# Kernel optimization log

Hardware: AMD Instinct MI355X
Metric: run time of the kernel (lower is better)

## Reference

```python
import jax, jax.numpy as jnp
import numpy as np

B, D3, DQ, H, UNITS, SK = 32, 1024, 1024, 1024, 1024, 1024


def setup_inputs() -> dict:
    key = jax.random.key(0)
    ks = jax.random.split(key, 11)
    return {
        "K": jax.random.normal(ks[0], (B, SK, UNITS), jnp.float32),
        "Q": jax.random.normal(ks[1], (B, DQ, D3), jnp.float32),
        "M": jax.random.normal(ks[2], (B, D3, D3), jnp.float32),
        "ht": jax.random.normal(ks[3], (B, D3, H), jnp.float32),
        "Wp": jax.random.normal(ks[4], (D3, DQ), jnp.float32) * 0.02,
        "bp": jax.random.normal(ks[5], (D3,), jnp.float32) * 0.02,
        "W3": jax.random.normal(ks[6], (D3, D3), jnp.float32) * 0.02,
        "W4": jax.random.normal(ks[7], (D3, D3), jnp.float32) * 0.02,
        "b3": jax.random.normal(ks[8], (D3,), jnp.float32) * 0.02,
        "Wd": jax.random.normal(ks[9], (H + D3, UNITS), jnp.float32) * 0.02,
        "bd": jax.random.normal(ks[10], (UNITS,), jnp.float32) * 0.02,
    }


def reference(K, Q, M, ht, Wp, bp, W3, W4, b3, Wd, bd):
    # q = Wp @ Q + bp  -> (B, d3, d3); bp broadcasts over the last axis
    q = jnp.einsum('ij,bjk->bik', Wp, Q) + bp
    # concat([ht, q], axis=-1) -> (B, d3, h + d3), then fresh Dense(units)
    concat = jnp.concatenate([ht, q], axis=-1)
    mlp = jnp.einsum('bdc,cu->bdu', concat, Wd) + bd  # (B, d3, units)
    # scores = K @ mlp^T, softmax over last axis (computed but unused in the
    # original layer's output -- kept for faithfulness; DCE'd under jit)
    scores = jnp.einsum('bsu,bdu->bsd', K, mlp)       # (B, sK, d3)
    distribution = jax.nn.softmax(scores, axis=-1)
    del distribution
    # Belta = relu(W3 @ M + W4 @ q + b3), gated multiply with q
    Belta = jax.nn.relu(
        jnp.einsum('ij,bjk->bik', W3, M)
        + jnp.einsum('ij,bjk->bik', W4, q)
        + b3
    )
    q_new = Belta * q  # (B, d3, d3)
    return q_new
```

## Files before the change

### kernel.cpp

```cpp
#include <hip/hip_runtime.h>
#include <stdint.h>


#define D_ 1024

typedef __attribute__((ext_vector_type(8))) short short8;
typedef __attribute__((ext_vector_type(4))) float floatx4;
typedef __attribute__((ext_vector_type(4))) unsigned short us4;

#define VMCNT0() asm volatile("s_waitcnt vmcnt(0)" ::: "memory")
#define VMCNT4() asm volatile("s_waitcnt vmcnt(4)" ::: "memory")
#define LGKM0()  asm volatile("s_waitcnt lgkmcnt(0)" ::: "memory")

__device__ __forceinline__ unsigned short f2bf(float f) {
  union { float f; unsigned int u; } v; v.f = f;
  unsigned int u = v.u;
  unsigned int r = (u + 0x7FFFu + ((u >> 16) & 1u)) >> 16;
  return (unsigned short)r;
}

__device__ __forceinline__ float bf2f(unsigned short h) {
  union { unsigned int u; float f; } v; v.u = ((unsigned int)h) << 16;
  return v.f;
}

__device__ __forceinline__ void async_load16(const void* g, void* l) {
  __builtin_amdgcn_global_load_lds(
      (const __attribute__((address_space(1))) unsigned int*)g,
      (__attribute__((address_space(3))) unsigned int*)l, 16, 0, 0);
}

__global__ __launch_bounds__(256) void transpose_cvt2(
    const float* __restrict__ in0, unsigned short* __restrict__ out0,
    const float* __restrict__ in1, unsigned short* __restrict__ out1) {
  __shared__ float tile[64][65];
  const int zz = blockIdx.z;
  const float* in = (zz < 32) ? in0 : in1;
  unsigned short* out = (zz < 32) ? out0 : out1;
  const int b = zz & 31;
  const long base = ((long)b) << 20;
  const int r0 = blockIdx.y * 64, c0 = blockIdx.x * 64;
  const int t = threadIdx.x;
  const int tr = t >> 4, tc4 = (t & 15) * 4;
#pragma unroll
  for (int p = 0; p < 4; ++p) {
    const int row = p * 16 + tr;
    const float4 v = *(const float4*)&in[base + (long)(r0 + row) * D_ + c0 + tc4];
    tile[row][tc4 + 0] = v.x; tile[row][tc4 + 1] = v.y;
    tile[row][tc4 + 2] = v.z; tile[row][tc4 + 3] = v.w;
  }
  __syncthreads();
#pragma unroll
  for (int p = 0; p < 4; ++p) {
    const int c = p * 16 + tr;
    us4 pk;
    pk.x = f2bf(tile[tc4 + 0][c]);
    pk.y = f2bf(tile[tc4 + 1][c]);
    pk.z = f2bf(tile[tc4 + 2][c]);
    pk.w = f2bf(tile[tc4 + 3][c]);
    *(us4*)&out[base + (long)(c0 + c) * D_ + r0 + tc4] = pk;
  }
}

__global__ __launch_bounds__(256) void convert_weights(
    const float* __restrict__ Wp, const float* __restrict__ W3,
    const float* __restrict__ W4, unsigned short* __restrict__ Wpb,
    unsigned short* __restrict__ A2) {
  const int i = blockIdx.x * 256 + threadIdx.x;
  const long e = (long)i * 4;
  const int row = (int)(e >> 10);
  const int col = (int)(e & 1023);
  const float4 a = ((const float4*)Wp)[i];
  us4 pa; pa.x = f2bf(a.x); pa.y = f2bf(a.y); pa.z = f2bf(a.z); pa.w = f2bf(a.w);
  ((us4*)Wpb)[i] = pa;
  const float4 w3 = ((const float4*)W3)[i];
  us4 p3; p3.x = f2bf(w3.x); p3.y = f2bf(w3.y); p3.z = f2bf(w3.z); p3.w = f2bf(w3.w);
  *(us4*)&A2[(long)row * 2048 + col] = p3;
  const float4 w4 = ((const float4*)W4)[i];
  us4 p4; p4.x = f2bf(w4.x); p4.y = f2bf(w4.y); p4.z = f2bf(w4.z); p4.w = f2bf(w4.w);
  *(us4*)&A2[(long)row * 2048 + 1024 + col] = p4;
}

template <int NT, int LDA, bool IS_G2>
__global__ __launch_bounds__(512, 2) void gemm8p(
    const unsigned short* __restrict__ A,
    const unsigned short* __restrict__ B1,
    const unsigned short* __restrict__ B2,
    const float* __restrict__ bias,
    void* __restrict__ outp) {
  __shared__ __align__(16) unsigned short As[2][256 * 64];
  __shared__ __align__(16) unsigned short Bs[2][256 * 64];

  const int lane = threadIdx.x & 63;
  const int w = threadIdx.x >> 6;
  const int wm = (w >> 2) * 128;
  const int wn = (w & 3) * 64;
  const int l15 = lane & 15;
  const int quad = lane >> 4;

  const int bid = blockIdx.x;
  const int swz = (bid & 7) * 64 + (bid >> 3);
  const int b = swz >> 4;
  const int m0 = ((swz >> 2) & 3) * 256;
  const int n0 = (swz & 3) * 256;
  const long bb = ((long)b) << 20;

  const int sr = lane >> 3;
  const int sc = ((lane & 7) ^ sr) * 8;

  const unsigned short* Ag = A + (long)(m0 + w * 16 + sr) * LDA + sc;
  const unsigned short* Bg1 = B1 + bb + (long)(n0 + w * 16 + sr) * D_ + sc;
  const unsigned short* Bg2 =
      B2 ? (B2 + bb + (long)(n0 + w * 16 + sr) * D_ + sc) : (const unsigned short*)0;

  const int kx0 = (quad * 16) ^ ((lane & 7) << 4);
  const int kx1 = (64 + quad * 16) ^ ((lane & 7) << 4);

  floatx4 acc[8][4] = {};

  auto stageAh = [&](int buf, int kt, int h) {
#pragma unroll
    for (int j = 0; j < 2; ++j)
      async_load16(Ag + (long)(h * 128 + j * 8) * LDA + (long)kt * 64,
                   &As[buf][(h * 128 + w * 16 + j * 8) * 64]);
  };
  auto stageBh = [&](int buf, int kt, int h) {
    const unsigned short* bs;
    if constexpr (IS_G2) {
      bs = (kt < 16) ? (Bg1 + (long)kt * 64) : (Bg2 + (long)(kt - 16) * 64);
    } else {
      bs = Bg1 + (long)kt * 64;
    }
#pragma unroll
    for (int j = 0; j < 2; ++j)
      async_load16(bs + (long)(h * 128 + j * 8) * D_,
                   &Bs[buf][(h * 128 + w * 16 + j * 8) * 64]);
  };

  auto ldA = [&](int buf, int fi, int kx) -> short8 {
    return *(const short8*)((const char*)&As[buf][0] +
                            (long)((wm + fi * 16 + l15) * 128 + kx));
  };
  auto ldB = [&](int buf, int fi, int kx) -> short8 {
    return *(const short8*)((const char*)&Bs[buf][0] +
                            (long)((wn + fi * 16 + l15) * 128 + kx));
  };

  stageAh(0, 0, 0); stageAh(0, 0, 1);
  stageBh(0, 0, 0); stageBh(0, 0, 1);
  stageBh(1, 1, 0); stageBh(1, 1, 1);
  VMCNT4();
  __builtin_amdgcn_s_barrier();

  short8 a[4][2], bq[4][2];

  auto tile = [&](int t, int buf) {
#pragma unroll
    for (int r = 0; r < 4; ++r) { a[r][0] = ldA(buf, r, kx0); a[r][1] = ldA(buf, r, kx1); }
#pragma unroll
    for (int c = 0; c < 2; ++c) { bq[c][0] = ldB(buf, c, kx0); bq[c][1] = ldB(buf, c, kx1); }
    if (t + 1 < NT) stageAh(buf ^ 1, t + 1, 0);
    __builtin_amdgcn_s_barrier();
    LGKM0();
    __builtin_amdgcn_sched_barrier(0);
    __builtin_amdgcn_s_setprio(1);
#pragma unroll
    for (int r = 0; r < 4; ++r)
#pragma unroll
      for (int c = 0; c < 2; ++c)
#pragma unroll
        for (int ks = 0; ks < 2; ++ks)
          acc[r][c] = __builtin_amdgcn_mfma_f32_16x16x32_bf16(
              a[r][ks], bq[c][ks], acc[r][c], 0, 0, 0);
    __builtin_amdgcn_s_setprio(0);
    __builtin_amdgcn_s_barrier();

#pragma unroll
    for (int c = 0; c < 2; ++c) { bq[2 + c][0] = ldB(buf, 2 + c, kx0); bq[2 + c][1] = ldB(buf, 2 + c, kx1); }
    if (t + 1 < NT) stageAh(buf ^ 1, t + 1, 1);
    __builtin_amdgcn_s_barrier();
    LGKM0();
    __builtin_amdgcn_sched_barrier(0);
    __builtin_amdgcn_s_setprio(1);
#pragma unroll
    for (int r = 0; r < 4; ++r)
#pragma unroll
      for (int c = 0; c < 2; ++c)
#pragma unroll
        for (int ks = 0; ks < 2; ++ks)
          acc[r][2 + c] = __builtin_amdgcn_mfma_f32_16x16x32_bf16(
              a[r][ks], bq[2 + c][ks], acc[r][2 + c], 0, 0, 0);
    __builtin_amdgcn_s_setprio(0);
    __builtin_amdgcn_s_barrier();

#pragma unroll
    for (int r = 0; r < 4; ++r) { a[r][0] = ldA(buf, 4 + r, kx0); a[r][1] = ldA(buf, 4 + r, kx1); }
    if (t + 2 < NT) stageBh(buf, t + 2, 0);
    __builtin_amdgcn_s_barrier();
    LGKM0();
    __builtin_amdgcn_sched_barrier(0);
    __builtin_amdgcn_s_setprio(1);
#pragma unroll
    for (int r = 0; r < 4; ++r)
#pragma unroll
      for (int c = 0; c < 2; ++c)
#pragma unroll
        for (int ks = 0; ks < 2; ++ks)
          acc[4 + r][2 + c] = __builtin_amdgcn_mfma_f32_16x16x32_bf16(
              a[r][ks], bq[2 + c][ks], acc[4 + r][2 + c], 0, 0, 0);
    __builtin_amdgcn_s_setprio(0);
    __builtin_amdgcn_s_barrier();

    if (t + 2 < NT) stageBh(buf, t + 2, 1);
    __builtin_amdgcn_s_barrier();
    __builtin_amdgcn_s_setprio(1);
#pragma unroll
    for (int r = 0; r < 4; ++r)
#pragma unroll
      for (int c = 0; c < 2; ++c)
#pragma unroll
        for (int ks = 0; ks < 2; ++ks)
          acc[4 + r][c] = __builtin_amdgcn_mfma_f32_16x16x32_bf16(
              a[r][ks], bq[c][ks], acc[4 + r][c], 0, 0, 0);
    __builtin_amdgcn_s_setprio(0);
    if (t < NT - 2) { VMCNT4(); } else { VMCNT0(); }
    __builtin_amdgcn_s_barrier();
  };

#pragma unroll 1
  for (int tt = 0; tt < NT; tt += 2) {
    tile(tt, 0);
    tile(tt + 1, 1);
  }

  if constexpr (!IS_G2) {
    unsigned short* qt = (unsigned short*)outp;
#pragma unroll
    for (int c = 0; c < 4; ++c) {
      const int col = n0 + wn + c * 16 + l15;
      const float bv = bias[col];
#pragma unroll
      for (int r = 0; r < 8; ++r) {
        const int row = m0 + wm + r * 16 + quad * 4;
        const floatx4 v = acc[r][c];
        us4 pk;
        pk.x = f2bf(v.x + bv); pk.y = f2bf(v.y + bv);
        pk.z = f2bf(v.z + bv); pk.w = f2bf(v.w + bv);
        *(us4*)&qt[bb + (long)col * D_ + row] = pk;
      }
    }
  } else {
    float* outv = (float*)outp;
#pragma unroll
    for (int c = 0; c < 4; ++c) {
      const int col = n0 + wn + c * 16 + l15;
      const float bv = bias[col];
#pragma unroll
      for (int r = 0; r < 8; ++r) {
        const int row = m0 + wm + r * 16 + quad * 4;
        const floatx4 v = acc[r][c];
        const us4 qv = *(const us4*)&B2[bb + (long)col * D_ + row];
        outv[bb + (long)(row + 0) * D_ + col] = fmaxf(v.x + bv, 0.0f) * bf2f(qv.x);
        outv[bb + (long)(row + 1) * D_ + col] = fmaxf(v.y + bv, 0.0f) * bf2f(qv.y);
        outv[bb + (long)(row + 2) * D_ + col] = fmaxf(v.z + bv, 0.0f) * bf2f(qv.z);
        outv[bb + (long)(row + 3) * D_ + col] = fmaxf(v.w + bv, 0.0f) * bf2f(qv.w);
      }
    }
  }
}

extern "C" void kernel_launch(void* const* d_in, const int* in_sizes, int n_in,
                              void* d_out, int out_size, void* d_ws, size_t ws_size,
                              hipStream_t stream) {
  const float* Q  = (const float*)d_in[1];
  const float* M  = (const float*)d_in[2];
  const float* Wp = (const float*)d_in[4];
  const float* bp = (const float*)d_in[5];
  const float* W3 = (const float*)d_in[6];
  const float* W4 = (const float*)d_in[7];
  const float* b3 = (const float*)d_in[8];
  float* out = (float*)d_out;

  char* ws = (char*)d_ws;
  unsigned short* qt  = (unsigned short*)(ws);
  unsigned short* Qt  = (unsigned short*)(ws + (64l  << 20));
  unsigned short* Mt  = (unsigned short*)(ws + (128l << 20));
  unsigned short* Wpb = (unsigned short*)(ws + (192l << 20));
  unsigned short* A2  = (unsigned short*)(ws + (194l << 20));

  dim3 tgrid(16, 16, 64);
  transpose_cvt2<<<tgrid, 256, 0, stream>>>(Q, Qt, M, Mt);
  convert_weights<<<1024, 256, 0, stream>>>(Wp, W3, W4, Wpb, A2);

  gemm8p<16, 1024, false><<<dim3(512), dim3(512), 0, stream>>>(
      Wpb, Qt, (const unsigned short*)nullptr, bp, qt);
  gemm8p<32, 2048, true><<<dim3(512), dim3(512), 0, stream>>>(
      A2, Mt, qt, b3, out);
}
```

Measured before the change: 689.1 us.

## Restructure GEMM main loop with ping-pong register fragments and whole-tile prefetch

Replaces the per-tile four-phase schedule with separate low and high A/B register fragment sets. LDS reads for the next quadrant or next k-tile are issued while the MFMAs of the current quadrant run, and quadrant order alternates between even and odd tiles so fragments are reused. Global-to-LDS staging now loads the whole A and B tile for t+2 at once, waiting with vmcnt(8) and then vmcnt(0), instead of staging A for t+1 and B for t+2 in halves. This aims to hide LDS latency behind matrix-core work, at the cost of more registers and a full vmcnt(0) wait in every tile.

```diff
diff --git a/kernel.cpp b/kernel.cpp
--- a/kernel.cpp
+++ b/kernel.cpp
@@ -9,8 +9,23 @@
 typedef __attribute__((ext_vector_type(4))) unsigned short us4;
 
 #define VMCNT0() asm volatile("s_waitcnt vmcnt(0)" ::: "memory")
-#define VMCNT4() asm volatile("s_waitcnt vmcnt(4)" ::: "memory")
+#define VMCNT8() asm volatile("s_waitcnt vmcnt(8)" ::: "memory")
 #define LGKM0()  asm volatile("s_waitcnt lgkmcnt(0)" ::: "memory")
+#define SCHED0() __builtin_amdgcn_sched_barrier(0)
+#define BAR()    __builtin_amdgcn_s_barrier()
+
+#define MQ(ASET, BSET, R0, C0)                                               \
+  do {                                                                       \
+    __builtin_amdgcn_s_setprio(1);                                           \
+    _Pragma("unroll") for (int r_ = 0; r_ < 4; ++r_)                         \
+        _Pragma("unroll") for (int c_ = 0; c_ < 2; ++c_)                     \
+            _Pragma("unroll") for (int k_ = 0; k_ < 2; ++k_)                 \
+                acc[(R0) + r_][(C0) + c_] =                                  \
+                    __builtin_amdgcn_mfma_f32_16x16x32_bf16(                 \
+                        ASET[r_][k_], BSET[c_][k_],                          \
+                        acc[(R0) + r_][(C0) + c_], 0, 0, 0);                 \
+    __builtin_amdgcn_s_setprio(0);                                           \
+  } while (0)
 
 __device__ __forceinline__ unsigned short f2bf(float f) {
   union { float f; unsigned int u; } v; v.f = f;
@@ -82,7 +97,7 @@
 }
 
 template <int NT, int LDA, bool IS_G2>
-__global__ __launch_bounds__(512, 2) void gemm8p(
+__global__ __launch_bounds__(512, 2) void gemmpl(
     const unsigned short* __restrict__ A,
     const unsigned short* __restrict__ B1,
     const unsigned short* __restrict__ B2,
@@ -117,14 +132,19 @@
   const int kx1 = (64 + quad * 16) ^ ((lane & 7) << 4);
 
   floatx4 acc[8][4] = {};
-
-  auto stageAh = [&](int buf, int kt, int h) {
-#pragma unroll
-    for (int j = 0; j < 2; ++j)
-      async_load16(Ag + (long)(h * 128 + j * 8) * LDA + (long)kt * 64,
-                   &As[buf][(h * 128 + w * 16 + j * 8) * 64]);
-  };
-  auto stageBh = [&](int buf, int kt, int h) {
+  short8 aLo[4][2], aHi[4][2], bLo[2][2], bHi[2][2];
+
+  auto stageA = [&](int kt) {
+    unsigned short* dst = &As[kt & 1][0];
+#pragma unroll
+    for (int h = 0; h < 2; ++h)
+#pragma unroll
+      for (int j = 0; j < 2; ++j)
+        async_load16(Ag + (long)(h * 128 + j * 8) * LDA + (long)kt * 64,
+                     dst + (h * 128 + w * 16 + j * 8) * 64);
+  };
+  auto stageB = [&](int kt) {
+    unsigned short* dst = &Bs[kt & 1][0];
     const unsigned short* bs;
     if constexpr (IS_G2) {
       bs = (kt < 16) ? (Bg1 + (long)kt * 64) : (Bg2 + (long)(kt - 16) * 64);
@@ -132,9 +152,11 @@
       bs = Bg1 + (long)kt * 64;
     }
 #pragma unroll
-    for (int j = 0; j < 2; ++j)
-      async_load16(bs + (long)(h * 128 + j * 8) * D_,
-                   &Bs[buf][(h * 128 + w * 16 + j * 8) * 64]);
+    for (int h = 0; h < 2; ++h)
+#pragma unroll
+      for (int j = 0; j < 2; ++j)
+        async_load16(bs + (long)(h * 128 + j * 8) * D_,
+                     dst + (h * 128 + w * 16 + j * 8) * 64);
   };
 
   auto ldA = [&](int buf, int fi, int kx) -> short8 {
@@ -146,91 +168,75 @@
                             (long)((wn + fi * 16 + l15) * 128 + kx));
   };
 
-  stageAh(0, 0, 0); stageAh(0, 0, 1);
-  stageBh(0, 0, 0); stageBh(0, 0, 1);
-  stageBh(1, 1, 0); stageBh(1, 1, 1);
-  VMCNT4();
-  __builtin_amdgcn_s_barrier();
-
-  short8 a[4][2], bq[4][2];
-
-  auto tile = [&](int t, int buf) {
-#pragma unroll
-    for (int r = 0; r < 4; ++r) { a[r][0] = ldA(buf, r, kx0); a[r][1] = ldA(buf, r, kx1); }
-#pragma unroll
-    for (int c = 0; c < 2; ++c) { bq[c][0] = ldB(buf, c, kx0); bq[c][1] = ldB(buf, c, kx1); }
-    if (t + 1 < NT) stageAh(buf ^ 1, t + 1, 0);
-    __builtin_amdgcn_s_barrier();
-    LGKM0();
-    __builtin_amdgcn_sched_barrier(0);
-    __builtin_amdgcn_s_setprio(1);
-#pragma unroll
-    for (int r = 0; r < 4; ++r)
-#pragma unroll
-      for (int c = 0; c < 2; ++c)
-#pragma unroll
-        for (int ks = 0; ks < 2; ++ks)
-          acc[r][c] = __builtin_amdgcn_mfma_f32_16x16x32_bf16(
-              a[r][ks], bq[c][ks], acc[r][c], 0, 0, 0);
-    __builtin_amdgcn_s_setprio(0);
-    __builtin_amdgcn_s_barrier();
-
-#pragma unroll
-    for (int c = 0; c < 2; ++c) { bq[2 + c][0] = ldB(buf, 2 + c, kx0); bq[2 + c][1] = ldB(buf, 2 + c, kx1); }
-    if (t + 1 < NT) stageAh(buf ^ 1, t + 1, 1);
-    __builtin_amdgcn_s_barrier();
-    LGKM0();
-    __builtin_amdgcn_sched_barrier(0);
-    __builtin_amdgcn_s_setprio(1);
-#pragma unroll
-    for (int r = 0; r < 4; ++r)
-#pragma unroll
-      for (int c = 0; c < 2; ++c)
-#pragma unroll
-        for (int ks = 0; ks < 2; ++ks)
-          acc[r][2 + c] = __builtin_amdgcn_mfma_f32_16x16x32_bf16(
-              a[r][ks], bq[2 + c][ks], acc[r][2 + c], 0, 0, 0);
-    __builtin_amdgcn_s_setprio(0);
-    __builtin_amdgcn_s_barrier();
-
-#pragma unroll
-    for (int r = 0; r < 4; ++r) { a[r][0] = ldA(buf, 4 + r, kx0); a[r][1] = ldA(buf, 4 + r, kx1); }
-    if (t + 2 < NT) stageBh(buf, t + 2, 0);
-    __builtin_amdgcn_s_barrier();
-    LGKM0();
-    __builtin_amdgcn_sched_barrier(0);
-    __builtin_amdgcn_s_setprio(1);
-#pragma unroll
-    for (int r = 0; r < 4; ++r)
-#pragma unroll
-      for (int c = 0; c < 2; ++c)
-#pragma unroll
-        for (int ks = 0; ks < 2; ++ks)
-          acc[4 + r][2 + c] = __builtin_amdgcn_mfma_f32_16x16x32_bf16(
-              a[r][ks], bq[2 + c][ks], acc[4 + r][2 + c], 0, 0, 0);
-    __builtin_amdgcn_s_setprio(0);
-    __builtin_amdgcn_s_barrier();
-
-    if (t + 2 < NT) stageBh(buf, t + 2, 1);
-    __builtin_amdgcn_s_barrier();
-    __builtin_amdgcn_s_setprio(1);
-#pragma unroll
-    for (int r = 0; r < 4; ++r)
-#pragma unroll
-      for (int c = 0; c < 2; ++c)
-#pragma unroll
-        for (int ks = 0; ks < 2; ++ks)
-          acc[4 + r][c] = __builtin_amdgcn_mfma_f32_16x16x32_bf16(
-              a[r][ks], bq[c][ks], acc[4 + r][c], 0, 0, 0);
-    __builtin_amdgcn_s_setprio(0);
-    if (t < NT - 2) { VMCNT4(); } else { VMCNT0(); }
-    __builtin_amdgcn_s_barrier();
+  auto rdALo = [&](int buf) {
+#pragma unroll
+    for (int r = 0; r < 4; ++r) { aLo[r][0] = ldA(buf, r, kx0); aLo[r][1] = ldA(buf, r, kx1); }
+  };
+  auto rdAHi = [&](int buf) {
+#pragma unroll
+    for (int r = 0; r < 4; ++r) { aHi[r][0] = ldA(buf, 4 + r, kx0); aHi[r][1] = ldA(buf, 4 + r, kx1); }
+  };
+  auto rdBLo = [&](int buf) {
+#pragma unroll
+    for (int c = 0; c < 2; ++c) { bLo[c][0] = ldB(buf, c, kx0); bLo[c][1] = ldB(buf, c, kx1); }
+  };
+  auto rdBHi = [&](int buf) {
+#pragma unroll
+    for (int c = 0; c < 2; ++c) { bHi[c][0] = ldB(buf, 2 + c, kx0); bHi[c][1] = ldB(buf, 2 + c, kx1); }
+  };
+
+  stageA(0); stageB(0);
+  stageA(1); stageB(1);
+  VMCNT8();
+  BAR();
+  rdALo(0); rdBLo(0);
+
+  auto tileEven = [&](int t) {
+    BAR(); LGKM0(); SCHED0();
+    rdBHi(0);
+    SCHED0();
+    MQ(aLo, bLo, 0, 0);
+    BAR(); LGKM0(); SCHED0();
+    rdAHi(0);
+    VMCNT0();
+    SCHED0();
+    MQ(aLo, bHi, 0, 2);
+    BAR(); LGKM0(); SCHED0();
+    if (t + 1 < NT) rdALo(1);
+    SCHED0();
+    MQ(aHi, bHi, 4, 2);
+    BAR(); LGKM0(); SCHED0();
+    if (t + 1 < NT) rdBHi(1);
+    if (t + 2 < NT) { stageA(t + 2); stageB(t + 2); }
+    SCHED0();
+    MQ(aHi, bLo, 4, 0);
+  };
+
+  auto tileOdd = [&](int t) {
+    BAR(); LGKM0(); SCHED0();
+    rdBLo(1);
+    SCHED0();
+    MQ(aLo, bHi, 0, 2);
+    BAR(); LGKM0(); SCHED0();
+    rdAHi(1);
+    VMCNT0();
+    SCHED0();
+    MQ(aLo, bLo, 0, 0);
+    BAR(); LGKM0(); SCHED0();
+    if (t + 1 < NT) rdALo(0);
+    SCHED0();
+    MQ(aHi, bLo, 4, 0);
+    BAR(); LGKM0(); SCHED0();
+    if (t + 1 < NT) rdBLo(0);
+    if (t + 2 < NT) { stageA(t + 2); stageB(t + 2); }
+    SCHED0();
+    MQ(aHi, bHi, 4, 2);
   };
 
 #pragma unroll 1
   for (int tt = 0; tt < NT; tt += 2) {
-    tile(tt, 0);
-    tile(tt + 1, 1);
+    tileEven(tt);
+    tileOdd(tt + 1);
   }
 
   if constexpr (!IS_G2) {
@@ -292,8 +298,8 @@
   transpose_cvt2<<<tgrid, 256, 0, stream>>>(Q, Qt, M, Mt);
   convert_weights<<<1024, 256, 0, stream>>>(Wp, W3, W4, Wpb, A2);
 
-  gemm8p<16, 1024, false><<<dim3(512), dim3(512), 0, stream>>>(
+  gemmpl<16, 1024, false><<<dim3(512), dim3(512), 0, stream>>>(
       Wpb, Qt, (const unsigned short*)nullptr, bp, qt);
-  gemm8p<32, 2048, true><<<dim3(512), dim3(512), 0, stream>>>(
+  gemmpl<32, 2048, true><<<dim3(512), dim3(512), 0, stream>>>(
       A2, Mt, qt, b3, out);
 }
```

New measurement: 674.2 us. -2.2%, faster.
